# Optimization experiments

Measured on AMD Instinct MI355X. Metric: run time of the kernel, lower is better.

## Reference

```python
import jax, jax.numpy as jnp
import numpy as np

B, S, D, H = 4, 2048, 1024, 16
HS = D // H          # head size 64
DF = 4 * D           # ffn hidden 4096
EPS = 1e-5


def _layer_norm(x, g, b):
    mu = jnp.mean(x, axis=-1, keepdims=True)
    var = jnp.var(x, axis=-1, keepdims=True)
    return (x - mu) * jax.lax.rsqrt(var + EPS) * g + b


def setup_inputs() -> dict:
    key = jax.random.key(0)
    ks = jax.random.split(key, 12)
    s_d = 1.0 / np.sqrt(D)
    s_f = 1.0 / np.sqrt(DF)
    return {
        "x": jax.random.normal(ks[0], (B, S, D), jnp.float32),
        # per-head q/k/v projections, batched over heads: [H, D, HS]
        "wq": jax.random.uniform(ks[1], (H, D, HS), jnp.float32, -s_d, s_d),
        "wk": jax.random.uniform(ks[2], (H, D, HS), jnp.float32, -s_d, s_d),
        "wv": jax.random.uniform(ks[3], (H, D, HS), jnp.float32, -s_d, s_d),
        "proj_w": jax.random.uniform(ks[4], (D, D), jnp.float32, -s_d, s_d),
        "proj_b": jax.random.uniform(ks[5], (D,), jnp.float32, -s_d, s_d),
        "ff1_w": jax.random.uniform(ks[6], (D, DF), jnp.float32, -s_d, s_d),
        "ff1_b": jax.random.uniform(ks[7], (DF,), jnp.float32, -s_d, s_d),
        "ff2_w": jax.random.uniform(ks[8], (DF, D), jnp.float32, -s_f, s_f),
        "ff2_b": jax.random.uniform(ks[9], (D,), jnp.float32, -s_f, s_f),
        "ln1_g": jnp.ones((D,), jnp.float32),
        "ln1_b": jnp.zeros((D,), jnp.float32),
        "ln2_g": jnp.ones((D,), jnp.float32),
        "ln2_b": jnp.zeros((D,), jnp.float32),
    }


def reference(x, wq, wk, wv, proj_w, proj_b, ff1_w, ff1_b, ff2_w, ff2_b,
              ln1_g, ln1_b, ln2_g, ln2_b):
    # --- multi-head causal self-attention on ln1(x), all heads batched ---
    h = _layer_norm(x, ln1_g, ln1_b)                      # [B,S,D]
    q = jnp.einsum("bsd,hde->bhse", h, wq)                # [B,H,S,HS]
    k = jnp.einsum("bsd,hde->bhse", h, wk)
    v = jnp.einsum("bsd,hde->bhse", h, wv)
    scale = HS ** -0.5
    scores = jnp.einsum("bhse,bhte->bhst", q, k) * scale  # [B,H,S,S]
    causal = jnp.tril(jnp.ones((S, S), bool))
    scores = jnp.where(causal, scores, jnp.finfo(scores.dtype).min)
    att = jax.nn.softmax(scores, axis=-1)
    o = jnp.einsum("bhst,bhte->bhse", att, v)             # [B,H,S,HS]
    o = o.transpose(0, 2, 1, 3).reshape(B, S, D)          # concat heads
    sa = o @ proj_w + proj_b
    x = x + sa
    # --- FFN on ln2(x) ---
    h2 = _layer_norm(x, ln2_g, ln2_b)
    ff = jax.nn.relu(h2 @ ff1_w + ff1_b) @ ff2_w + ff2_b
    return x + ff
```

## Files before the change

### kernel.cpp

```cpp
#include <hip/hip_runtime.h>
#include <hip/hip_bf16.h>

#define BB 4
#define SS 2048
#define DD 1024
#define HH 16
#define HSZ 64
#define DFF 4096

typedef short short8 __attribute__((ext_vector_type(8)));
typedef float f32x4 __attribute__((ext_vector_type(4)));
typedef unsigned short us4 __attribute__((ext_vector_type(4)));

#define AS1 __attribute__((address_space(1)))
#define AS3 __attribute__((address_space(3)))

__device__ __forceinline__ unsigned short f2bf(float f) {
    return __bfloat16_as_ushort(__float2bfloat16(f));
}

__global__ __launch_bounds__(256) void pack_qkv_kernel(
    const float* __restrict__ wq, const float* __restrict__ wk,
    const float* __restrict__ wv, __hip_bfloat16* __restrict__ out)
{
    __shared__ float tile[64][65];
    const int bid = blockIdx.x;
    const int kt = bid & 15, hh = (bid >> 4) & 15, sel = bid >> 8;
    const float* src = (sel == 0) ? wq : (sel == 1) ? wk : wv;
    src += (size_t)hh * (DD * HSZ) + (size_t)kt * 64 * HSZ;
    const int tx = threadIdx.x & 63, ty = threadIdx.x >> 6;
    #pragma unroll
    for (int r = 0; r < 64; r += 4)
        tile[r + ty][tx] = src[(size_t)(r + ty) * HSZ + tx];
    __syncthreads();
    unsigned short* o = (unsigned short*)out + (size_t)(sel * DD + hh * 64) * DD + kt * 64;
    #pragma unroll
    for (int r = 0; r < 64; r += 4) {
        int e = r + ty;
        o[(size_t)e * DD + tx] = f2bf(tile[tx][e]);
    }
}

__global__ __launch_bounds__(256) void pack_T_kernel(
    const float* __restrict__ in, __hip_bfloat16* __restrict__ out, int K, int N)
{
    __shared__ float tile[64][65];
    const int nb = N >> 6;
    const int tn0 = (blockIdx.x % nb) << 6, tk0 = (blockIdx.x / nb) << 6;
    const int tx = threadIdx.x & 63, ty = threadIdx.x >> 6;
    #pragma unroll
    for (int r = 0; r < 64; r += 4)
        tile[r + ty][tx] = in[(size_t)(tk0 + r + ty) * N + tn0 + tx];
    __syncthreads();
    unsigned short* o = (unsigned short*)out;
    #pragma unroll
    for (int r = 0; r < 64; r += 4) {
        int n = r + ty;
        o[(size_t)(tn0 + n) * K + tk0 + tx] = f2bf(tile[tx][n]);
    }
}

__global__ __launch_bounds__(256) void ln_kernel(
    const float* __restrict__ x, const float* __restrict__ g,
    const float* __restrict__ b, __hip_bfloat16* __restrict__ out)
{
    int row = blockIdx.x;
    int t = threadIdx.x;
    const float4* xr = (const float4*)(x + (size_t)row * DD);
    float4 v = xr[t];
    float s = v.x + v.y + v.z + v.w;
    float ss = v.x * v.x + v.y * v.y + v.z * v.z + v.w * v.w;
    #pragma unroll
    for (int off = 32; off; off >>= 1) {
        s += __shfl_xor(s, off, 64);
        ss += __shfl_xor(ss, off, 64);
    }
    __shared__ float red[8];
    int w = t >> 6, lane = t & 63;
    if (lane == 0) { red[w] = s; red[4 + w] = ss; }
    __syncthreads();
    s = red[0] + red[1] + red[2] + red[3];
    ss = red[4] + red[5] + red[6] + red[7];
    float mu = s * (1.f / DD);
    float var = ss * (1.f / DD) - mu * mu;
    float rs = rsqrtf(var + 1e-5f);
    float4 gv = ((const float4*)g)[t];
    float4 bv = ((const float4*)b)[t];
    ushort4 pk = make_ushort4(
        f2bf((v.x - mu) * rs * gv.x + bv.x),
        f2bf((v.y - mu) * rs * gv.y + bv.y),
        f2bf((v.z - mu) * rs * gv.z + bv.z),
        f2bf((v.w - mu) * rs * gv.w + bv.w));
    *(ushort4*)((unsigned short*)out + (size_t)row * DD + t * 4) = pk;
}

template<int BN, bool BIAS, bool RELU, bool RES, bool OUTF32>
__global__ __launch_bounds__(512) void gemm_kernel(
    const __hip_bfloat16* __restrict__ A, const __hip_bfloat16* __restrict__ BT,
    const float* __restrict__ bias, const float* __restrict__ res,
    void* __restrict__ Cout, int M, int N, int K, int nbx)
{
    constexpr int NB = BN / 128;
    constexpr int NREP = BN / 64;
    __shared__ uint4 Ah[2][2][1024];
    __shared__ uint4 Bh[2][NB][1024];

    const int tid = threadIdx.x;
    const int lane = tid & 63;
    const int w = tid >> 6;
    const int lr = lane & 15, g = lane >> 4;
    const int nwg = gridDim.x;
    const int cpx = nwg >> 3;
    const int wg = blockIdx.x;
    const int swz = (wg & 7) * cpx + (wg >> 3);
    const int bx = swz % nbx, by = swz / nbx;
    const int row0 = by * 256, col0 = bx * BN;
    const int wm = w >> 2, wn = w & 3;
    const int NT = K >> 6;

    f32x4 acc0[4][NREP] = {};
    f32x4 acc1[4][NREP] = {};
    short8 bfr[NREP][2];

    auto stageA = [&](int buf, int half, int t) {
        const int k0 = t * 64;
        #pragma unroll
        for (int j = 0; j < 2; ++j) {
            int s = j * 512 + tid;
            int r = s >> 3;
            int c = (s & 7) ^ (r & 7);
            const __hip_bfloat16* src = A + (size_t)(row0 + half * 128 + r) * K + k0 + c * 8;
            __builtin_amdgcn_global_load_lds((const AS1 void*)src,
                (AS3 void*)(&Ah[buf][half][j * 512 + (tid & ~63)]), 16, 0, 0);
        }
    };
    auto stageB = [&](int buf, int half, int t) {
        const int k0 = t * 64;
        #pragma unroll
        for (int j = 0; j < 2; ++j) {
            int s = j * 512 + tid;
            int r = s >> 3;
            int c = (s & 7) ^ (r & 7);
            const __hip_bfloat16* src = BT + (size_t)(col0 + half * 128 + r) * K + k0 + c * 8;
            __builtin_amdgcn_global_load_lds((const AS1 void*)src,
                (AS3 void*)(&Bh[buf][half][j * 512 + (tid & ~63)]), 16, 0, 0);
        }
    };
    auto loadB = [&](int buf) {
        const int hb = (NB == 2) ? (wn >> 1) : 0;
        const int cb = (NB == 2) ? ((wn & 1) * 64) : (wn * 32);
        #pragma unroll
        for (int n = 0; n < NREP; ++n) {
            int c = cb + n * 16 + lr;
            #pragma unroll
            for (int kk = 0; kk < 2; ++kk)
                bfr[n][kk] = *(const short8*)&Bh[buf][hb][c * 8 + ((kk * 4 + g) ^ (c & 7))];
        }
    };
    auto phase = [&](auto& acc, int buf, int mh) {
        short8 af[4][2];
        #pragma unroll
        for (int mi = 0; mi < 4; ++mi) {
            int r = wm * 64 + mi * 16 + lr;
            #pragma unroll
            for (int kk = 0; kk < 2; ++kk)
                af[mi][kk] = *(const short8*)&Ah[buf][mh][r * 8 + ((kk * 4 + g) ^ (r & 7))];
        }
        asm volatile("s_waitcnt lgkmcnt(0)" ::: "memory");
        __builtin_amdgcn_sched_barrier(0);
        __builtin_amdgcn_s_setprio(1);
        #pragma unroll
        for (int mi = 0; mi < 4; ++mi)
            #pragma unroll
            for (int n = 0; n < NREP; ++n)
                #pragma unroll
                for (int kk = 0; kk < 2; ++kk)
                    acc[mi][n] = __builtin_amdgcn_mfma_f32_16x16x32_bf16(
                        af[mi][kk], bfr[n][kk], acc[mi][n], 0, 0, 0);
        __builtin_amdgcn_s_setprio(0);
    };

    stageA(0, 0, 0);
    stageB(0, 0, 0);
    if constexpr (NB == 2) stageB(0, 1, 0);
    stageA(0, 1, 0);
    stageA(1, 0, 1);
    if constexpr (NB == 2) stageB(1, 0, 1);

    for (int t = 0; t < NT; ++t) {
        const int buf = t & 1;
        if (t < NT - 1) {
            if constexpr (NB == 2) asm volatile("s_waitcnt vmcnt(4)" ::: "memory");
            else                   asm volatile("s_waitcnt vmcnt(2)" ::: "memory");
        } else {
            asm volatile("s_waitcnt vmcnt(0)" ::: "memory");
        }
        __builtin_amdgcn_s_barrier();
        __builtin_amdgcn_sched_barrier(0);
        if (t + 1 < NT) {
            if constexpr (NB == 2) { stageB(buf ^ 1, 1, t + 1); stageA(buf ^ 1, 1, t + 1); }
            else                   { stageB(buf ^ 1, 0, t + 1); stageA(buf ^ 1, 1, t + 1); }
        }
        loadB(buf);
        phase(acc0, buf, 0);
        if (t < NT - 1) {
            if constexpr (NB == 2) asm volatile("s_waitcnt vmcnt(8)" ::: "memory");
            else                   asm volatile("s_waitcnt vmcnt(6)" ::: "memory");
        } else {
            asm volatile("s_waitcnt vmcnt(0)" ::: "memory");
        }
        __builtin_amdgcn_s_barrier();
        __builtin_amdgcn_sched_barrier(0);
        if (t + 2 < NT) {
            stageA(buf, 0, t + 2);
            if constexpr (NB == 2) stageB(buf, 0, t + 2);
        }
        phase(acc1, buf, 1);
    }

    auto store = [&](auto& acc, int mh) {
        #pragma unroll
        for (int mi = 0; mi < 4; ++mi) {
            #pragma unroll
            for (int j = 0; j < 4; ++j) {
                int rr = row0 + mh * 128 + wm * 64 + mi * 16 + g * 4 + j;
                #pragma unroll
                for (int n = 0; n < NREP; ++n) {
                    int cc = col0 + wn * (NREP * 16) + n * 16 + lr;
                    float vv = acc[mi][n][j];
                    if (BIAS) vv += bias[cc];
                    if (RELU) vv = fmaxf(vv, 0.f);
                    if (RES) vv += res[(size_t)rr * N + cc];
                    if (OUTF32) ((float*)Cout)[(size_t)rr * N + cc] = vv;
                    else ((__hip_bfloat16*)Cout)[(size_t)rr * N + cc] = __float2bfloat16(vv);
                }
            }
        }
    };
    store(acc0, 0);
    store(acc1, 1);
}

__device__ __forceinline__ void stage_kv(
    const unsigned short* __restrict__ qkvu, size_t rowbase, int h, int kv0, int tl,
    unsigned short* __restrict__ Kb, unsigned short* __restrict__ Vb)
{
    {
        int kv = tl >> 2, c = tl & 3;
        const unsigned short* src = qkvu + rowbase + (size_t)(kv0 + kv) * 3072 + DD + h * HSZ + c * 16;
        uint4 v0 = *(const uint4*)src;
        uint4 v1 = *(const uint4*)(src + 8);
        int sw = kv & 7;
        *(uint4*)&Kb[kv * 64 + ((2 * c) ^ sw) * 8] = v0;
        *(uint4*)&Kb[kv * 64 + ((2 * c + 1) ^ sw) * 8] = v1;
    }
    {
        int bkv = ((tl >> 6) << 2) | (tl & 3);
        int bd = (tl >> 2) & 15;
        const unsigned short* src = qkvu + rowbase + (size_t)(kv0 + bkv * 4) * 3072 + 2 * DD + h * HSZ + bd * 4;
        us4 r0 = *(const us4*)src;
        us4 r1 = *(const us4*)(src + 3072);
        us4 r2 = *(const us4*)(src + 2 * 3072);
        us4 r3 = *(const us4*)(src + 3 * 3072);
        #pragma unroll
        for (int cc = 0; cc < 4; ++cc) {
            int d = bd * 4 + cc;
            us4 wv = { r0[cc], r1[cc], r2[cc], r3[cc] };
            *(us4*)&Vb[d * 64 + (((bkv >> 1) ^ (d & 7)) * 8) + (bkv & 1) * 4] = wv;
        }
    }
}

__device__ __forceinline__ void flash_tile(
    const unsigned short* __restrict__ Kb, const unsigned short* __restrict__ Vb,
    unsigned short* __restrict__ Pw, const short8* qfc, int qgc, int kv0, int q, int g,
    float& m_run, float& l_run, f32x4* oacc, bool masked)
{
    f32x4 st[4] = {};
    __builtin_amdgcn_s_setprio(1);
    #pragma unroll
    for (int tt = 0; tt < 4; ++tt) {
        #pragma unroll
        for (int kk = 0; kk < 2; ++kk) {
            short8 kf = *(const short8*)&Kb[(tt * 16 + q) * 64 + ((4 * kk + g) ^ (q & 7)) * 8];
            st[tt] = __builtin_amdgcn_mfma_f32_16x16x32_bf16(kf, qfc[kk], st[tt], 0, 0, 0);
        }
    }
    __builtin_amdgcn_s_setprio(0);

    const float SC = 0.1803368801111731f;
    float mt = -1e30f;
    if (masked) {
        #pragma unroll
        for (int tt = 0; tt < 4; ++tt)
            #pragma unroll
            for (int j = 0; j < 4; ++j) {
                float s = st[tt][j] * SC;
                int kvg = kv0 + tt * 16 + g * 4 + j;
                s = (kvg <= qgc) ? s : -1e30f;
                st[tt][j] = s;
                mt = fmaxf(mt, s);
            }
    } else {
        #pragma unroll
        for (int tt = 0; tt < 4; ++tt)
            #pragma unroll
            for (int j = 0; j < 4; ++j) {
                float s = st[tt][j] * SC;
                st[tt][j] = s;
                mt = fmaxf(mt, s);
            }
    }
    mt = fmaxf(mt, __shfl_xor(mt, 16, 64));
    mt = fmaxf(mt, __shfl_xor(mt, 32, 64));

    bool defer = __all(mt <= m_run + 11.0f);
    if (!defer) {
        float m_new = fmaxf(m_run, mt);
        float corr = exp2f(m_run - m_new);
        #pragma unroll
        for (int j = 0; j < 4; ++j) {
            float cj = __shfl(corr, g * 4 + j, 64);
            #pragma unroll
            for (int dn = 0; dn < 4; ++dn)
                oacc[dn][j] *= cj;
        }
        l_run *= corr;
        m_run = m_new;
    }

    float lsum = 0.f;
    #pragma unroll
    for (int tt = 0; tt < 4; ++tt)
        #pragma unroll
        for (int j = 0; j < 4; ++j) {
            float p = exp2f(st[tt][j] - m_run);
            st[tt][j] = p;
            lsum += p;
        }
    lsum += __shfl_xor(lsum, 16, 64);
    lsum += __shfl_xor(lsum, 32, 64);
    l_run += lsum;

    __builtin_amdgcn_s_setprio(1);
    #pragma unroll
    for (int kk = 0; kk < 2; ++kk) {
        #pragma unroll
        for (int rt = 0; rt < 2; ++rt) {
            int tt = kk * 2 + rt;
            unsigned int lo = ((unsigned int)f2bf(st[tt][1]) << 16) | (unsigned int)f2bf(st[tt][0]);
            unsigned int hi = ((unsigned int)f2bf(st[tt][3]) << 16) | (unsigned int)f2bf(st[tt][2]);
            uint2 pk = make_uint2(lo, hi);
            *(uint2*)&Pw[q * 32 + ((2 * rt + (g >> 1)) ^ ((q >> 1) & 3)) * 8 + (g & 1) * 4] = pk;
        }
        short8 pf = *(const short8*)&Pw[q * 32 + (g ^ ((q >> 1) & 3)) * 8];
        #pragma unroll
        for (int dn = 0; dn < 4; ++dn) {
            short8 vf = *(const short8*)&Vb[(dn * 16 + q) * 64 + ((4 * kk + g) ^ (q & 7)) * 8];
            oacc[dn] = __builtin_amdgcn_mfma_f32_16x16x32_bf16(pf, vf, oacc[dn], 0, 0, 0);
        }
    }
    __builtin_amdgcn_s_setprio(0);
}

__global__ __launch_bounds__(512, 4) void attn_kernel(
    const __hip_bfloat16* __restrict__ qkv, __hip_bfloat16* __restrict__ o)
{
    __shared__ unsigned short K_lds[2][64 * 64];
    __shared__ unsigned short Vt_lds[2][64 * 64];
    __shared__ unsigned short P_lds[8 * 512];

    const int t = threadIdx.x;
    const int lane = t & 63, w = t >> 6;
    const int grp = w >> 2, wq4 = w & 3, tl = t & 255;
    const int q = lane & 15, g = lane >> 4;
    const int pq = blockIdx.x & 15;
    const int h = (blockIdx.x >> 4) & 15;
    const int b = blockIdx.x >> 8;
    const int qtA = pq, qtB = 31 - pq;
    const int qt1 = grp ? qtB : qtA;
    const unsigned short* qkvu = (const unsigned short*)qkv;
    const size_t rowbase = (size_t)(b * SS) * 3072;
    unsigned short* Kb = K_lds[grp];
    unsigned short* Vb = Vt_lds[grp];
    unsigned short* Pw = &P_lds[w * 512];
    unsigned short* op = (unsigned short*)o;

    int qt_cur = qt1;
    int qgc = qt_cur * 64 + wq4 * 16 + q;
    short8 qfc[2];
    #pragma unroll
    for (int kk = 0; kk < 2; ++kk)
        qfc[kk] = *(const short8*)(qkvu + rowbase + (size_t)qgc * 3072 + h * HSZ + kk * 32 + g * 8);

    f32x4 oacc[4] = {};
    float m_run = -1e30f, l_run = 0.f;

    for (int it = 0; it <= pq; ++it) {
        __syncthreads();
        stage_kv(qkvu, rowbase, h, it * 64, tl, Kb, Vb);
        __syncthreads();
        flash_tile(Kb, Vb, Pw, qfc, qgc, it * 64, q, g, m_run, l_run, oacc, it == qt_cur);
    }

    if (grp == 0) {
        #pragma unroll
        for (int j = 0; j < 4; ++j) {
            float lj = __shfl(l_run, g * 4 + j, 64);
            float inv = 1.f / lj;
            int orow = qtA * 64 + wq4 * 16 + g * 4 + j;
            #pragma unroll
            for (int dn = 0; dn < 4; ++dn)
                op[(size_t)(b * SS + orow) * DD + h * HSZ + dn * 16 + q] = f2bf(oacc[dn][j] * inv);
        }
        qt_cur = qtB;
        qgc = qtB * 64 + wq4 * 16 + q;
        #pragma unroll
        for (int kk = 0; kk < 2; ++kk)
            qfc[kk] = *(const short8*)(qkvu + rowbase + (size_t)qgc * 3072 + h * HSZ + kk * 32 + g * 8);
        m_run = -1e30f; l_run = 0.f;
        #pragma unroll
        for (int dn = 0; dn < 4; ++dn) oacc[dn] = f32x4{0.f, 0.f, 0.f, 0.f};
    }

    for (int it2 = 0; it2 < 16 - pq; ++it2) {
        int tile = grp ? (pq + 1 + it2) : (16 + it2);
        bool active = grp ? (tile <= 15) : true;
        __syncthreads();
        if (active) stage_kv(qkvu, rowbase, h, tile * 64, tl, Kb, Vb);
        __syncthreads();
        if (active) flash_tile(Kb, Vb, Pw, qfc, qgc, tile * 64, q, g, m_run, l_run, oacc,
                               tile == qt_cur);
    }

    __syncthreads();
    float* obuf = (float*)K_lds;
    float* mlbuf = (float*)P_lds;
    if (grp == 0) {
        #pragma unroll
        for (int dn = 0; dn < 4; ++dn)
            #pragma unroll
            for (int j = 0; j < 4; ++j)
                obuf[wq4 * 1024 + lane * 16 + dn * 4 + j] = oacc[dn][j];
        if (g == 0) { mlbuf[wq4 * 32 + q] = m_run; mlbuf[wq4 * 32 + 16 + q] = l_run; }
    }
    __syncthreads();
    if (grp == 1) {
        float mA = mlbuf[wq4 * 32 + q];
        float lA = mlbuf[wq4 * 32 + 16 + q];
        float mM = fmaxf(m_run, mA);
        float sB = exp2f(m_run - mM);
        float sA = exp2f(mA - mM);
        float lM = l_run * sB + lA * sA;
        #pragma unroll
        for (int j = 0; j < 4; ++j) {
            float sBj = __shfl(sB, g * 4 + j, 64);
            float sAj = __shfl(sA, g * 4 + j, 64);
            float lMj = __shfl(lM, g * 4 + j, 64);
            float inv = 1.f / lMj;
            int orow = qtB * 64 + wq4 * 16 + g * 4 + j;
            #pragma unroll
            for (int dn = 0; dn < 4; ++dn) {
                float oA = obuf[wq4 * 1024 + lane * 16 + dn * 4 + j];
                float vv = (oacc[dn][j] * sBj + oA * sAj) * inv;
                op[(size_t)(b * SS + orow) * DD + h * HSZ + dn * 16 + q] = f2bf(vv);
            }
        }
    }
}

extern "C" void kernel_launch(void* const* d_in, const int* in_sizes, int n_in,
                              void* d_out, int out_size, void* d_ws, size_t ws_size,
                              hipStream_t stream)
{
    const float* x      = (const float*)d_in[0];
    const float* wq     = (const float*)d_in[1];
    const float* wk     = (const float*)d_in[2];
    const float* wv     = (const float*)d_in[3];
    const float* proj_w = (const float*)d_in[4];
    const float* proj_b = (const float*)d_in[5];
    const float* ff1_w  = (const float*)d_in[6];
    const float* ff1_b  = (const float*)d_in[7];
    const float* ff2_w  = (const float*)d_in[8];
    const float* ff2_b  = (const float*)d_in[9];
    const float* ln1_g  = (const float*)d_in[10];
    const float* ln1_b  = (const float*)d_in[11];
    const float* ln2_g  = (const float*)d_in[12];
    const float* ln2_b  = (const float*)d_in[13];
    float* out = (float*)d_out;

    char* ws = (char*)d_ws;
    const size_t MB = 1ull << 20;
    __hip_bfloat16* h     = (__hip_bfloat16*)(ws);
    __hip_bfloat16* qkv   = (__hip_bfloat16*)(ws + 16 * MB);
    __hip_bfloat16* obuf  = (__hip_bfloat16*)(ws + 64 * MB);
    float*          x1    = (float*)(ws + 80 * MB);
    __hip_bfloat16* wqkvT = (__hip_bfloat16*)(ws + 112 * MB);
    __hip_bfloat16* projT = (__hip_bfloat16*)(ws + 118 * MB);
    __hip_bfloat16* ff1T  = (__hip_bfloat16*)(ws + 120 * MB);
    __hip_bfloat16* ff2T  = (__hip_bfloat16*)(ws + 128 * MB);
    __hip_bfloat16* f1    = (__hip_bfloat16*)(ws + 16 * MB);

    const int ROWS = BB * SS;

    pack_qkv_kernel<<<768, 256, 0, stream>>>(wq, wk, wv, wqkvT);
    pack_T_kernel<<<(DD / 64) * (DD / 64), 256, 0, stream>>>(proj_w, projT, DD, DD);
    pack_T_kernel<<<(DFF / 64) * (DD / 64), 256, 0, stream>>>(ff1_w, ff1T, DD, DFF);
    pack_T_kernel<<<(DD / 64) * (DFF / 64), 256, 0, stream>>>(ff2_w, ff2T, DFF, DD);

    ln_kernel<<<ROWS, 256, 0, stream>>>(x, ln1_g, ln1_b, h);
    gemm_kernel<128, false, false, false, false><<<(ROWS / 256) * (3 * DD / 128), 512, 0, stream>>>(
        h, wqkvT, nullptr, nullptr, qkv, ROWS, 3 * DD, DD, 3 * DD / 128);
    attn_kernel<<<BB * HH * 16, 512, 0, stream>>>(qkv, obuf);
    gemm_kernel<128, true, false, true, true><<<(ROWS / 256) * (DD / 128), 512, 0, stream>>>(
        obuf, projT, proj_b, x, x1, ROWS, DD, DD, DD / 128);
    ln_kernel<<<ROWS, 256, 0, stream>>>(x1, ln2_g, ln2_b, h);
    gemm_kernel<256, true, true, false, false><<<(ROWS / 256) * (DFF / 256), 512, 0, stream>>>(
        h, ff1T, ff1_b, nullptr, f1, ROWS, DFF, DD, DFF / 256);
    gemm_kernel<128, true, false, true, true><<<(ROWS / 256) * (DD / 128), 512, 0, stream>>>(
        f1, ff2T, ff2_b, x1, out, ROWS, DD, DFF, DD / 128);
}
```

Baseline: 422.3 us.

## Split GEMM into 256- and 128-wide kernels with finer-grained staging phases

Replaces the templated GEMM with two specialised kernels. The 256-wide kernel gives each wave a 128x64 sub-tile and splits each K-step into four phases, issuing A and B staging loads one half-tile at a time between barriers. The 128-wide kernel uses a 4x2 wave grid with 64x64 sub-tiles and splits work along K instead of M. The QKV GEMM now uses the 256-wide tile, which halves its grid. The aim is more data reuse per wave and better overlap of global loads with MFMA work, at the cost of more barriers, higher register pressure and fewer workgroups for the QKV GEMM.

Result: slower. 456.3 us (+8.0%).

```diff
diff --git a/kernel.cpp b/kernel.cpp
--- a/kernel.cpp
+++ b/kernel.cpp
@@ -94,77 +94,182 @@
     *(ushort4*)((unsigned short*)out + (size_t)row * DD + t * 4) = pk;
 }
 
-template<int BN, bool BIAS, bool RELU, bool RES, bool OUTF32>
-__global__ __launch_bounds__(512) void gemm_kernel(
+template<bool BIAS, bool RELU, bool RES, bool OUTF32>
+__global__ __launch_bounds__(512) void gemm256_kernel(
     const __hip_bfloat16* __restrict__ A, const __hip_bfloat16* __restrict__ BT,
     const float* __restrict__ bias, const float* __restrict__ res,
     void* __restrict__ Cout, int M, int N, int K, int nbx)
 {
-    constexpr int NB = BN / 128;
-    constexpr int NREP = BN / 64;
     __shared__ uint4 Ah[2][2][1024];
-    __shared__ uint4 Bh[2][NB][1024];
-
-    const int tid = threadIdx.x;
-    const int lane = tid & 63;
-    const int w = tid >> 6;
+    __shared__ uint4 Bh[2][2][1024];
+    const int tid = threadIdx.x, lane = tid & 63, w = tid >> 6;
     const int lr = lane & 15, g = lane >> 4;
-    const int nwg = gridDim.x;
-    const int cpx = nwg >> 3;
-    const int wg = blockIdx.x;
+    const int nwg = gridDim.x, cpx = nwg >> 3, wg = blockIdx.x;
     const int swz = (wg & 7) * cpx + (wg >> 3);
     const int bx = swz % nbx, by = swz / nbx;
-    const int row0 = by * 256, col0 = bx * BN;
+    const int row0 = by * 256, col0 = bx * 256;
     const int wm = w >> 2, wn = w & 3;
     const int NT = K >> 6;
-
-    f32x4 acc0[4][NREP] = {};
-    f32x4 acc1[4][NREP] = {};
-    short8 bfr[NREP][2];
-
-    auto stageA = [&](int buf, int half, int t) {
+    f32x4 acc[8][4] = {};
+    short8 bfr[4][2];
+
+    auto stA = [&](int buf, int half, int t) {
         const int k0 = t * 64;
         #pragma unroll
         for (int j = 0; j < 2; ++j) {
             int s = j * 512 + tid;
-            int r = s >> 3;
-            int c = (s & 7) ^ (r & 7);
+            int r = s >> 3, c = (s & 7) ^ (r & 7);
             const __hip_bfloat16* src = A + (size_t)(row0 + half * 128 + r) * K + k0 + c * 8;
             __builtin_amdgcn_global_load_lds((const AS1 void*)src,
                 (AS3 void*)(&Ah[buf][half][j * 512 + (tid & ~63)]), 16, 0, 0);
         }
     };
-    auto stageB = [&](int buf, int half, int t) {
+    auto stB = [&](int buf, int half, int t) {
         const int k0 = t * 64;
         #pragma unroll
         for (int j = 0; j < 2; ++j) {
             int s = j * 512 + tid;
-            int r = s >> 3;
-            int c = (s & 7) ^ (r & 7);
+            int r = s >> 3, c = (s & 7) ^ (r & 7);
             const __hip_bfloat16* src = BT + (size_t)(col0 + half * 128 + r) * K + k0 + c * 8;
             __builtin_amdgcn_global_load_lds((const AS1 void*)src,
                 (AS3 void*)(&Bh[buf][half][j * 512 + (tid & ~63)]), 16, 0, 0);
         }
     };
     auto loadB = [&](int buf) {
-        const int hb = (NB == 2) ? (wn >> 1) : 0;
-        const int cb = (NB == 2) ? ((wn & 1) * 64) : (wn * 32);
-        #pragma unroll
-        for (int n = 0; n < NREP; ++n) {
-            int c = cb + n * 16 + lr;
+        #pragma unroll
+        for (int n = 0; n < 4; ++n) {
+            int cb = wn * 64 + n * 16 + lr;
+            int hb = cb >> 7, rr = cb & 127;
             #pragma unroll
             for (int kk = 0; kk < 2; ++kk)
-                bfr[n][kk] = *(const short8*)&Bh[buf][hb][c * 8 + ((kk * 4 + g) ^ (c & 7))];
-        }
-    };
-    auto phase = [&](auto& acc, int buf, int mh) {
-        short8 af[4][2];
+                bfr[n][kk] = *(const short8*)&Bh[buf][hb][rr * 8 + ((kk * 4 + g) ^ (rr & 7))];
+        }
+    };
+    auto phase = [&](int buf, int p) {
+        short8 af[2][2];
+        #pragma unroll
+        for (int m2 = 0; m2 < 2; ++m2) {
+            int rr = p * 32 + m2 * 16 + lr;
+            #pragma unroll
+            for (int kk = 0; kk < 2; ++kk)
+                af[m2][kk] = *(const short8*)&Ah[buf][wm][rr * 8 + ((kk * 4 + g) ^ (rr & 7))];
+        }
+        asm volatile("s_waitcnt lgkmcnt(0)" ::: "memory");
+        __builtin_amdgcn_sched_barrier(0);
+        __builtin_amdgcn_s_setprio(1);
+        #pragma unroll
+        for (int m2 = 0; m2 < 2; ++m2)
+            #pragma unroll
+            for (int n = 0; n < 4; ++n)
+                #pragma unroll
+                for (int kk = 0; kk < 2; ++kk)
+                    acc[p * 2 + m2][n] = __builtin_amdgcn_mfma_f32_16x16x32_bf16(
+                        af[m2][kk], bfr[n][kk], acc[p * 2 + m2][n], 0, 0, 0);
+        __builtin_amdgcn_s_setprio(0);
+    };
+
+    stB(0, 0, 0); stB(0, 1, 0);
+    stA(0, 0, 0); stA(0, 1, 0);
+    stB(1, 0, 1); stB(1, 1, 1);
+
+    for (int t = 0; t < NT; ++t) {
+        const int buf = t & 1;
+        if (t + 1 < NT) asm volatile("s_waitcnt vmcnt(4)" ::: "memory");
+        else            asm volatile("s_waitcnt vmcnt(0)" ::: "memory");
+        __builtin_amdgcn_s_barrier();
+        __builtin_amdgcn_sched_barrier(0);
+        if (t + 1 < NT) stA(buf ^ 1, 0, t + 1);
+        loadB(buf);
+        phase(buf, 0);
+        __builtin_amdgcn_s_barrier();
+        __builtin_amdgcn_sched_barrier(0);
+        if (t + 1 < NT) stA(buf ^ 1, 1, t + 1);
+        phase(buf, 1);
+        __builtin_amdgcn_s_barrier();
+        __builtin_amdgcn_sched_barrier(0);
+        if (t + 2 < NT) stB(buf, 0, t + 2);
+        phase(buf, 2);
+        __builtin_amdgcn_s_barrier();
+        __builtin_amdgcn_sched_barrier(0);
+        if (t + 2 < NT) stB(buf, 1, t + 2);
+        phase(buf, 3);
+    }
+
+    #pragma unroll
+    for (int mi = 0; mi < 8; ++mi) {
+        #pragma unroll
+        for (int j = 0; j < 4; ++j) {
+            int rr = row0 + wm * 128 + mi * 16 + g * 4 + j;
+            #pragma unroll
+            for (int n = 0; n < 4; ++n) {
+                int cc = col0 + wn * 64 + n * 16 + lr;
+                float vv = acc[mi][n][j];
+                if (BIAS) vv += bias[cc];
+                if (RELU) vv = fmaxf(vv, 0.f);
+                if (RES) vv += res[(size_t)rr * N + cc];
+                if (OUTF32) ((float*)Cout)[(size_t)rr * N + cc] = vv;
+                else ((__hip_bfloat16*)Cout)[(size_t)rr * N + cc] = __float2bfloat16(vv);
+            }
+        }
+    }
+}
+
+template<bool BIAS, bool RELU, bool RES, bool OUTF32>
+__global__ __launch_bounds__(512) void gemm128_kernel(
+    const __hip_bfloat16* __restrict__ A, const __hip_bfloat16* __restrict__ BT,
+    const float* __restrict__ bias, const float* __restrict__ res,
+    void* __restrict__ Cout, int M, int N, int K, int nbx)
+{
+    __shared__ uint4 Ah[2][2][1024];
+    __shared__ uint4 Bh[2][1024];
+    const int tid = threadIdx.x, lane = tid & 63, w = tid >> 6;
+    const int lr = lane & 15, g = lane >> 4;
+    const int nwg = gridDim.x, cpx = nwg >> 3, wg = blockIdx.x;
+    const int swz = (wg & 7) * cpx + (wg >> 3);
+    const int bx = swz % nbx, by = swz / nbx;
+    const int row0 = by * 256, col0 = bx * 128;
+    const int wm = w >> 1, wn = w & 1;
+    const int NT = K >> 6;
+    f32x4 acc[4][4] = {};
+    short8 bfr[4][2];
+
+    auto stA = [&](int buf, int half, int t) {
+        const int k0 = t * 64;
+        #pragma unroll
+        for (int j = 0; j < 2; ++j) {
+            int s = j * 512 + tid;
+            int r = s >> 3, c = (s & 7) ^ (r & 7);
+            const __hip_bfloat16* src = A + (size_t)(row0 + half * 128 + r) * K + k0 + c * 8;
+            __builtin_amdgcn_global_load_lds((const AS1 void*)src,
+                (AS3 void*)(&Ah[buf][half][j * 512 + (tid & ~63)]), 16, 0, 0);
+        }
+    };
+    auto stB = [&](int buf, int t) {
+        const int k0 = t * 64;
+        #pragma unroll
+        for (int j = 0; j < 2; ++j) {
+            int s = j * 512 + tid;
+            int r = s >> 3, c = (s & 7) ^ (r & 7);
+            const __hip_bfloat16* src = BT + (size_t)(col0 + r) * K + k0 + c * 8;
+            __builtin_amdgcn_global_load_lds((const AS1 void*)src,
+                (AS3 void*)(&Bh[buf][j * 512 + (tid & ~63)]), 16, 0, 0);
+        }
+    };
+    auto loadB = [&](int buf) {
+        #pragma unroll
+        for (int n = 0; n < 4; ++n) {
+            int cb = wn * 64 + n * 16 + lr;
+            #pragma unroll
+            for (int kk = 0; kk < 2; ++kk)
+                bfr[n][kk] = *(const short8*)&Bh[buf][cb * 8 + ((kk * 4 + g) ^ (cb & 7))];
+        }
+    };
+    auto phase = [&](int buf, int kk) {
+        short8 af[4];
         #pragma unroll
         for (int mi = 0; mi < 4; ++mi) {
             int r = wm * 64 + mi * 16 + lr;
-            #pragma unroll
-            for (int kk = 0; kk < 2; ++kk)
-                af[mi][kk] = *(const short8*)&Ah[buf][mh][r * 8 + ((kk * 4 + g) ^ (r & 7))];
+            af[mi] = *(const short8*)&Ah[buf][r >> 7][(r & 127) * 8 + ((kk * 4 + g) ^ (r & 7))];
         }
         asm volatile("s_waitcnt lgkmcnt(0)" ::: "memory");
         __builtin_amdgcn_sched_barrier(0);
@@ -172,73 +277,49 @@
         #pragma unroll
         for (int mi = 0; mi < 4; ++mi)
             #pragma unroll
-            for (int n = 0; n < NREP; ++n)
-                #pragma unroll
-                for (int kk = 0; kk < 2; ++kk)
-                    acc[mi][n] = __builtin_amdgcn_mfma_f32_16x16x32_bf16(
-                        af[mi][kk], bfr[n][kk], acc[mi][n], 0, 0, 0);
+            for (int n = 0; n < 4; ++n)
+                acc[mi][n] = __builtin_amdgcn_mfma_f32_16x16x32_bf16(
+                    af[mi], bfr[n][kk], acc[mi][n], 0, 0, 0);
         __builtin_amdgcn_s_setprio(0);
     };
 
-    stageA(0, 0, 0);
-    stageB(0, 0, 0);
-    if constexpr (NB == 2) stageB(0, 1, 0);
-    stageA(0, 1, 0);
-    stageA(1, 0, 1);
-    if constexpr (NB == 2) stageB(1, 0, 1);
+    stB(0, 0);
+    stA(0, 0, 0); stA(0, 1, 0);
+    stB(1, 1);
 
     for (int t = 0; t < NT; ++t) {
         const int buf = t & 1;
-        if (t < NT - 1) {
-            if constexpr (NB == 2) asm volatile("s_waitcnt vmcnt(4)" ::: "memory");
-            else                   asm volatile("s_waitcnt vmcnt(2)" ::: "memory");
-        } else {
-            asm volatile("s_waitcnt vmcnt(0)" ::: "memory");
-        }
+        if (t + 1 < NT) asm volatile("s_waitcnt vmcnt(2)" ::: "memory");
+        else            asm volatile("s_waitcnt vmcnt(0)" ::: "memory");
         __builtin_amdgcn_s_barrier();
         __builtin_amdgcn_sched_barrier(0);
-        if (t + 1 < NT) {
-            if constexpr (NB == 2) { stageB(buf ^ 1, 1, t + 1); stageA(buf ^ 1, 1, t + 1); }
-            else                   { stageB(buf ^ 1, 0, t + 1); stageA(buf ^ 1, 1, t + 1); }
-        }
+        if (t + 1 < NT) stA(buf ^ 1, 0, t + 1);
         loadB(buf);
-        phase(acc0, buf, 0);
-        if (t < NT - 1) {
-            if constexpr (NB == 2) asm volatile("s_waitcnt vmcnt(8)" ::: "memory");
-            else                   asm volatile("s_waitcnt vmcnt(6)" ::: "memory");
-        } else {
-            asm volatile("s_waitcnt vmcnt(0)" ::: "memory");
-        }
+        phase(buf, 0);
         __builtin_amdgcn_s_barrier();
         __builtin_amdgcn_sched_barrier(0);
-        if (t + 2 < NT) {
-            stageA(buf, 0, t + 2);
-            if constexpr (NB == 2) stageB(buf, 0, t + 2);
-        }
-        phase(acc1, buf, 1);
-    }
-
-    auto store = [&](auto& acc, int mh) {
-        #pragma unroll
-        for (int mi = 0; mi < 4; ++mi) {
-            #pragma unroll
-            for (int j = 0; j < 4; ++j) {
-                int rr = row0 + mh * 128 + wm * 64 + mi * 16 + g * 4 + j;
-                #pragma unroll
-                for (int n = 0; n < NREP; ++n) {
-                    int cc = col0 + wn * (NREP * 16) + n * 16 + lr;
-                    float vv = acc[mi][n][j];
-                    if (BIAS) vv += bias[cc];
-                    if (RELU) vv = fmaxf(vv, 0.f);
-                    if (RES) vv += res[(size_t)rr * N + cc];
-                    if (OUTF32) ((float*)Cout)[(size_t)rr * N + cc] = vv;
-                    else ((__hip_bfloat16*)Cout)[(size_t)rr * N + cc] = __float2bfloat16(vv);
-                }
+        if (t + 1 < NT) stA(buf ^ 1, 1, t + 1);
+        if (t + 2 < NT) stB(buf, t + 2);
+        phase(buf, 1);
+    }
+
+    #pragma unroll
+    for (int mi = 0; mi < 4; ++mi) {
+        #pragma unroll
+        for (int j = 0; j < 4; ++j) {
+            int rr = row0 + wm * 64 + mi * 16 + g * 4 + j;
+            #pragma unroll
+            for (int n = 0; n < 4; ++n) {
+                int cc = col0 + wn * 64 + n * 16 + lr;
+                float vv = acc[mi][n][j];
+                if (BIAS) vv += bias[cc];
+                if (RELU) vv = fmaxf(vv, 0.f);
+                if (RES) vv += res[(size_t)rr * N + cc];
+                if (OUTF32) ((float*)Cout)[(size_t)rr * N + cc] = vv;
+                else ((__hip_bfloat16*)Cout)[(size_t)rr * N + cc] = __float2bfloat16(vv);
             }
         }
-    };
-    store(acc0, 0);
-    store(acc1, 1);
+    }
 }
 
 __device__ __forceinline__ void stage_kv(
@@ -509,14 +590,14 @@
     pack_T_kernel<<<(DD / 64) * (DFF / 64), 256, 0, stream>>>(ff2_w, ff2T, DFF, DD);
 
     ln_kernel<<<ROWS, 256, 0, stream>>>(x, ln1_g, ln1_b, h);
-    gemm_kernel<128, false, false, false, false><<<(ROWS / 256) * (3 * DD / 128), 512, 0, stream>>>(
-        h, wqkvT, nullptr, nullptr, qkv, ROWS, 3 * DD, DD, 3 * DD / 128);
+    gemm256_kernel<false, false, false, false><<<(ROWS / 256) * (3 * DD / 256), 512, 0, stream>>>(
+        h, wqkvT, nullptr, nullptr, qkv, ROWS, 3 * DD, DD, 3 * DD / 256);
     attn_kernel<<<BB * HH * 16, 512, 0, stream>>>(qkv, obuf);
-    gemm_kernel<128, true, false, true, true><<<(ROWS / 256) * (DD / 128), 512, 0, stream>>>(
+    gemm128_kernel<true, false, true, true><<<(ROWS / 256) * (DD / 128), 512, 0, stream>>>(
         obuf, projT, proj_b, x, x1, ROWS, DD, DD, DD / 128);
     ln_kernel<<<ROWS, 256, 0, stream>>>(x1, ln2_g, ln2_b, h);
-    gemm_kernel<256, true, true, false, false><<<(ROWS / 256) * (DFF / 256), 512, 0, stream>>>(
+    gemm256_kernel<true, true, false, false><<<(ROWS / 256) * (DFF / 256), 512, 0, stream>>>(
         h, ff1T, ff1_b, nullptr, f1, ROWS, DFF, DD, DFF / 256);
-    gemm_kernel<128, true, false, true, true><<<(ROWS / 256) * (DD / 128), 512, 0, stream>>>(
+    gemm128_kernel<true, false, true, true><<<(ROWS / 256) * (DD / 128), 512, 0, stream>>>(
         f1, ff2T, ff2_b, x1, out, ROWS, DD, DFF, DD / 128);
 }
```
